# Performance work log

Hardware: AMD Instinct MI355X
Metric: run time of the kernel (lower is better)

The kernel has to match this reference:

```python
import jax, jax.numpy as jnp
import numpy as np

D_MAX = 4                      # max_displacement
OUT_DIM = 2 * D_MAX + 1        # 9 -> 9**3 = 729 displacement offsets


def setup_inputs() -> dict:
    key = jax.random.key(0)
    k1, k2 = jax.random.split(key)
    shape = (1, 32, 48, 48, 48)  # (N, C, H, W, D)
    x1 = jax.random.normal(k1, shape, dtype=jnp.float32)
    x2 = jax.random.normal(k2, shape, dtype=jnp.float32)
    return {"x1": x1, "x2": x2}


def _correlation(x1, x2):
    N, C, H, W, D = x1.shape
    p = D_MAX
    # zero-pad x2 on all three spatial dims (matches F.pad([pad]*6))
    x2p = jnp.pad(x2, ((0, 0), (0, 0), (p, p), (p, p), (p, p)))
    # offsets in the same order as the torch triple loop: i (H) slowest, k (D) fastest
    r = jnp.arange(OUT_DIM)
    offs = jnp.stack(jnp.meshgrid(r, r, r, indexing="ij"), axis=-1).reshape(-1, 3)  # (729, 3)

    def corr_one(o):
        sl = jax.lax.dynamic_slice(x2p, (0, 0, o[0], o[1], o[2]), (N, C, H, W, D))
        return jnp.mean(x1 * sl, axis=1)  # (N, H, W, D) — mean over channels

    cv = jax.vmap(corr_one)(offs)          # (729, N, H, W, D)
    return jnp.transpose(cv, (1, 0, 2, 3, 4))  # (N, 729, H, W, D)


def reference(x1, x2):
    return _correlation(x1, x2)
```

## Files before the change

kernel.cpp:

```cpp
#include <hip/hip_runtime.h>
#include <stdint.h>


#define HH 48
#define WW 48
#define DD 48
#define PAD 4
#define OD 9
#define WT 4
#define PP 8
#define NDG 6
#define CCH 8
#define NCHUNK 4
#define X2ROW 56
#define X2W 12
#define NACT 216
#define X2_UNITS 1344
#define X1_UNITS 384

__global__ __launch_bounds__(256, 2) void corr_kernel(
    const float* __restrict__ x1,
    const float* __restrict__ x2,
    float* __restrict__ out) {

  __shared__ __attribute__((aligned(16))) float s_x2[CCH * X2W * X2ROW];
  __shared__ __attribute__((aligned(16))) float s_x1[CCH * WT * DD];

  const int wt = blockIdx.x;
  const int h  = blockIdx.y;
  const int i  = blockIdx.z;
  const int w0 = wt * WT;
  const int r  = h + i - PAD;
  const int t  = threadIdx.x;
  const bool row_ok = (r >= 0) & (r < HH);

  const bool active = (t < NACT);
  int wl = 0, j = 0, dg = 0;
  if (active) {
    wl = t / (OD * NDG);
    int rem = t - wl * (OD * NDG);
    j = rem / NDG;
    dg = rem - j * NDG;
  }
  const int d0 = dg * PP;

  float acc[OD][PP];
#pragma unroll
  for (int k = 0; k < OD; ++k)
#pragma unroll
    for (int p = 0; p < PP; ++p) acc[k][p] = 0.0f;

  const int rbase = r * (WW * DD);

  for (int ch = 0; ch < NCHUNK; ++ch) {
    const int cbase = ch * CCH;

    float4 v2[6];
#pragma unroll
    for (int u = 0; u < 6; ++u) {
      const int idx = t + u * 256;
      const bool have = (u < 5) || (idx < X2_UNITS);
      const int c   = idx / 168;
      const int rm  = idx - c * 168;
      const int w   = rm / 14;
      const int pos = rm - w * 14;
      const int wg  = w0 + w - PAD;
      float4 val = make_float4(0.f, 0.f, 0.f, 0.f);
      const bool in = have & row_ok & ((unsigned)wg < (unsigned)WW) &
                      ((unsigned)(pos - 1) < 12u);
      if (in) {
        const size_t g = (size_t)(cbase + c) * (HH * WW * DD) + rbase +
                         wg * DD + (pos - 1) * 4;
        val = *reinterpret_cast<const float4*>(x2 + g);
      }
      v2[u] = val;
    }
    float4 v1[2];
#pragma unroll
    for (int u = 0; u < 2; ++u) {
      const int idx = t + u * 256;
      const bool have = (u < 1) || (idx < X1_UNITS);
      float4 val = make_float4(0.f, 0.f, 0.f, 0.f);
      if (have) {
        const int c   = idx / 48;
        const int lin = idx - c * 48;
        const size_t g = (size_t)(cbase + c) * (HH * WW * DD) +
                         (size_t)h * (WW * DD) + w0 * DD + lin * 4;
        val = *reinterpret_cast<const float4*>(x1 + g);
      }
      v1[u] = val;
    }

    __syncthreads();

#pragma unroll
    for (int u = 0; u < 6; ++u) {
      const int idx = t + u * 256;
      if ((u < 5) || (idx < X2_UNITS))
        *reinterpret_cast<float4*>(s_x2 + idx * 4) = v2[u];
    }
#pragma unroll
    for (int u = 0; u < 2; ++u) {
      const int idx = t + u * 256;
      if ((u < 1) || (idx < X1_UNITS))
        *reinterpret_cast<float4*>(s_x1 + idx * 4) = v1[u];
    }
    __syncthreads();

    if (active) {
      for (int c = 0; c < CCH; ++c) {
        float xv[PP];
        const float* px1 = &s_x1[c * (WT * DD) + wl * DD + d0];
#pragma unroll
        for (int p = 0; p < PP; ++p) xv[p] = px1[p];
        float win[PP + 8];
        const float* px2 = &s_x2[c * (X2W * X2ROW) + (wl + j) * X2ROW + d0];
#pragma unroll
        for (int q = 0; q < PP + 8; ++q) win[q] = px2[q];
#pragma unroll
        for (int k = 0; k < OD; ++k)
#pragma unroll
          for (int p = 0; p < PP; ++p)
            acc[k][p] = fmaf(xv[p], win[p + k], acc[k][p]);
      }
    }
  }

  if (active) {
    const float inv = 1.0f / 32.0f;
    const size_t spat = ((size_t)h * WW + (w0 + wl)) * DD + d0;
#pragma unroll
    for (int k = 0; k < OD; ++k) {
      const int o = (i * OD + j) * OD + k;
      float4 lo = make_float4(acc[k][0] * inv, acc[k][1] * inv,
                              acc[k][2] * inv, acc[k][3] * inv);
      float4 hi = make_float4(acc[k][4] * inv, acc[k][5] * inv,
                              acc[k][6] * inv, acc[k][7] * inv);
      float* dst = out + (size_t)o * (HH * WW * DD) + spat;
      *reinterpret_cast<float4*>(dst)     = lo;
      *reinterpret_cast<float4*>(dst + 4) = hi;
    }
  }
}

extern "C" void kernel_launch(void* const* d_in, const int* in_sizes, int n_in,
                              void* d_out, int out_size, void* d_ws, size_t ws_size,
                              hipStream_t stream) {
  const float* x1 = (const float*)d_in[0];
  const float* x2 = (const float*)d_in[1];
  float* out = (float*)d_out;
  dim3 grid(WW / WT, HH, OD);
  corr_kernel<<<grid, 256, 0, stream>>>(x1, x2, out);
}
```

Measured before the change: 395.7 us.

## Prefetch next channel chunk into registers during compute and pad x2 smem rows

Precomputes the per-thread global offsets and validity masks once, then issues the loads for the next channel chunk right after the shared-memory store so they overlap the FMA loop. It also widens the x2 shared-memory row from 56 to 60 floats (15 float4 per row), likely to reduce bank conflicts, and raises launch_bounds min blocks to 3. The risk is higher register pressure from the prefetch buffers plus the tighter register cap, which may cause spills.

```diff
diff --git a/kernel.cpp b/kernel.cpp
--- a/kernel.cpp
+++ b/kernel.cpp
@@ -12,13 +12,16 @@
 #define NDG 6
 #define CCH 8
 #define NCHUNK 4
-#define X2ROW 56
+#define X2ROW 60
+#define X2POS 15
 #define X2W 12
 #define NACT 216
-#define X2_UNITS 1344
+#define X2_UNITS 1440
 #define X1_UNITS 384
+#define HWD (HH * WW * DD)
+#define CHSTRIDE (CCH * HWD)
 
-__global__ __launch_bounds__(256, 2) void corr_kernel(
+__global__ __launch_bounds__(256, 3) void corr_kernel(
     const float* __restrict__ x1,
     const float* __restrict__ x2,
     float* __restrict__ out) {
@@ -44,53 +47,55 @@
   }
   const int d0 = dg * PP;
 
+  const int rbase = r * (WW * DD);
+  uint32_t o2[6];
+  bool in2[6];
+#pragma unroll
+  for (int u = 0; u < 6; ++u) {
+    const int idx = t + u * 256;
+    const bool have = (u < 5) || (idx < X2_UNITS);
+    const int c   = idx / (X2W * X2POS);
+    const int rm  = idx - c * (X2W * X2POS);
+    const int w   = rm / X2POS;
+    const int pos = rm - w * X2POS;
+    const int wg  = w0 + w - PAD;
+    in2[u] = have & row_ok & ((unsigned)wg < (unsigned)WW) &
+             ((unsigned)(pos - 1) < 12u);
+    o2[u] = (uint32_t)(c * HWD + rbase + wg * DD + (pos - 1) * 4);
+  }
+  uint32_t o1[2];
+  bool in1[2];
+#pragma unroll
+  for (int u = 0; u < 2; ++u) {
+    const int idx = t + u * 256;
+    in1[u] = (u < 1) || (idx < X1_UNITS);
+    const int c   = idx / 48;
+    const int lin = idx - c * 48;
+    o1[u] = (uint32_t)(c * HWD + h * (WW * DD) + w0 * DD + lin * 4);
+  }
+
   float acc[OD][PP];
 #pragma unroll
   for (int k = 0; k < OD; ++k)
 #pragma unroll
     for (int p = 0; p < PP; ++p) acc[k][p] = 0.0f;
 
-  const int rbase = r * (WW * DD);
+  float4 v2[6], v1[2];
+#pragma unroll
+  for (int u = 0; u < 6; ++u) {
+    float4 val = make_float4(0.f, 0.f, 0.f, 0.f);
+    if (in2[u]) val = *reinterpret_cast<const float4*>(x2 + o2[u]);
+    v2[u] = val;
+  }
+#pragma unroll
+  for (int u = 0; u < 2; ++u) {
+    float4 val = make_float4(0.f, 0.f, 0.f, 0.f);
+    if (in1[u]) val = *reinterpret_cast<const float4*>(x1 + o1[u]);
+    v1[u] = val;
+  }
 
+#pragma unroll
   for (int ch = 0; ch < NCHUNK; ++ch) {
-    const int cbase = ch * CCH;
-
-    float4 v2[6];
-#pragma unroll
-    for (int u = 0; u < 6; ++u) {
-      const int idx = t + u * 256;
-      const bool have = (u < 5) || (idx < X2_UNITS);
-      const int c   = idx / 168;
-      const int rm  = idx - c * 168;
-      const int w   = rm / 14;
-      const int pos = rm - w * 14;
-      const int wg  = w0 + w - PAD;
-      float4 val = make_float4(0.f, 0.f, 0.f, 0.f);
-      const bool in = have & row_ok & ((unsigned)wg < (unsigned)WW) &
-                      ((unsigned)(pos - 1) < 12u);
-      if (in) {
-        const size_t g = (size_t)(cbase + c) * (HH * WW * DD) + rbase +
-                         wg * DD + (pos - 1) * 4;
-        val = *reinterpret_cast<const float4*>(x2 + g);
-      }
-      v2[u] = val;
-    }
-    float4 v1[2];
-#pragma unroll
-    for (int u = 0; u < 2; ++u) {
-      const int idx = t + u * 256;
-      const bool have = (u < 1) || (idx < X1_UNITS);
-      float4 val = make_float4(0.f, 0.f, 0.f, 0.f);
-      if (have) {
-        const int c   = idx / 48;
-        const int lin = idx - c * 48;
-        const size_t g = (size_t)(cbase + c) * (HH * WW * DD) +
-                         (size_t)h * (WW * DD) + w0 * DD + lin * 4;
-        val = *reinterpret_cast<const float4*>(x1 + g);
-      }
-      v1[u] = val;
-    }
-
     __syncthreads();
 
 #pragma unroll
@@ -106,6 +111,23 @@
         *reinterpret_cast<float4*>(s_x1 + idx * 4) = v1[u];
     }
     __syncthreads();
+
+    if (ch + 1 < NCHUNK) {
+      const float* b2 = x2 + (size_t)(ch + 1) * CHSTRIDE;
+      const float* b1 = x1 + (size_t)(ch + 1) * CHSTRIDE;
+#pragma unroll
+      for (int u = 0; u < 6; ++u) {
+        float4 val = make_float4(0.f, 0.f, 0.f, 0.f);
+        if (in2[u]) val = *reinterpret_cast<const float4*>(b2 + o2[u]);
+        v2[u] = val;
+      }
+#pragma unroll
+      for (int u = 0; u < 2; ++u) {
+        float4 val = make_float4(0.f, 0.f, 0.f, 0.f);
+        if (in1[u]) val = *reinterpret_cast<const float4*>(b1 + o1[u]);
+        v1[u] = val;
+      }
+    }
 
     if (active) {
       for (int c = 0; c < CCH; ++c) {
```

Result: slower. 428.7 us (+8.3%).

## Double-buffer channel chunks via direct global-to-LDS async loads

Applied to the files above, without the earlier changes.

Replaces the register-staged global→LDS copy with AMD global_load_lds direct transfers into a double-buffered shared tile, prefetching the next channel chunk while the current one is computed. Chunk size halves to 4 channels, the shared buffers are zero-filled once so the padding halo stays zero, and hand-placed vmcnt waits plus raw barriers replace __syncthreads. It also widens LDS reads to float4 and raises the occupancy hint to 3 blocks. This aims to hide global load latency and cut register pressure, but relies on tricky manual waitcnt counts and per-wave load mapping.

```diff
diff --git a/kernel.cpp b/kernel.cpp
--- a/kernel.cpp
+++ b/kernel.cpp
@@ -10,21 +10,29 @@
 #define WT 4
 #define PP 8
 #define NDG 6
-#define CCH 8
-#define NCHUNK 4
-#define X2ROW 56
+#define CCH 4
+#define NCHUNK 8
+#define X2POS 15
+#define X2ROW 60
 #define X2W 12
 #define NACT 216
-#define X2_UNITS 1344
-#define X1_UNITS 384
+#define X2_FLOATS (CCH * X2W * X2ROW)
+#define X1_FLOATS (CCH * WT * DD)
+#define HWD (HH * WW * DD)
+#define CHFLOATS (CCH * HWD)
 
-__global__ __launch_bounds__(256, 2) void corr_kernel(
+#define GLOAD16(gp, lp)                                                  \
+  __builtin_amdgcn_global_load_lds(                                      \
+      (const __attribute__((address_space(1))) void*)(gp),               \
+      (__attribute__((address_space(3))) void*)(lp), 16, 0, 0)
+
+__global__ __launch_bounds__(256, 3) void corr_kernel(
     const float* __restrict__ x1,
     const float* __restrict__ x2,
     float* __restrict__ out) {
 
-  __shared__ __attribute__((aligned(16))) float s_x2[CCH * X2W * X2ROW];
-  __shared__ __attribute__((aligned(16))) float s_x1[CCH * WT * DD];
+  __shared__ __attribute__((aligned(16))) float s_x2[2][X2_FLOATS];
+  __shared__ __attribute__((aligned(16))) float s_x1[2][X1_FLOATS];
 
   const int wt = blockIdx.x;
   const int h  = blockIdx.y;
@@ -32,7 +40,38 @@
   const int w0 = wt * WT;
   const int r  = h + i - PAD;
   const int t  = threadIdx.x;
+  const int lane = t & 63;
+  const int wv   = t >> 6;
   const bool row_ok = (r >= 0) & (r < HH);
+
+  {
+    const float4 z = make_float4(0.f, 0.f, 0.f, 0.f);
+    float* p2 = &s_x2[0][0];
+    for (int s = t; s < (2 * X2_FLOATS) / 4; s += 256)
+      reinterpret_cast<float4*>(p2)[s] = z;
+    float* p1 = &s_x1[0][0];
+    for (int s = t; s < (2 * X1_FLOATS) / 4; s += 256)
+      reinterpret_cast<float4*>(p1)[s] = z;
+  }
+
+  uint32_t o2[3];
+  bool m2[3];
+#pragma unroll
+  for (int u = 0; u < 3; ++u) {
+    const int m   = u * 64 + lane;
+    const int w   = m / 15;
+    const int pos = m - w * 15;
+    const int wg  = w0 + w - PAD;
+    m2[u] = (m < 180) & row_ok & ((unsigned)wg < (unsigned)WW) &
+            ((unsigned)(pos - 1) < 12u);
+    o2[u] = (uint32_t)(wv * HWD + r * (WW * DD) + wg * DD + (pos - 1) * 4);
+  }
+  const bool m1 = (lane < 48);
+  const uint32_t o1 = (uint32_t)(wv * HWD + h * (WW * DD) + w0 * DD + lane * 4);
+
+  int nvm = 1;
+#pragma unroll
+  for (int u = 0; u < 3; ++u) nvm += (__ballot(m2[u]) != 0ull) ? 1 : 0;
 
   const bool active = (t < NACT);
   int wl = 0, j = 0, dg = 0;
@@ -50,73 +89,53 @@
 #pragma unroll
     for (int p = 0; p < PP; ++p) acc[k][p] = 0.0f;
 
-  const int rbase = r * (WW * DD);
+  __syncthreads();
+
+#pragma unroll
+  for (int u = 0; u < 3; ++u)
+    if (m2[u]) GLOAD16(x2 + o2[u], &s_x2[0][(wv * 180 + u * 64) * 4]);
+  if (m1) GLOAD16(x1 + o1, &s_x1[0][(wv * 48) * 4]);
 
   for (int ch = 0; ch < NCHUNK; ++ch) {
-    const int cbase = ch * CCH;
-
-    float4 v2[6];
+    const int b = ch & 1;
+    if (ch + 1 < NCHUNK) {
+      const float* g2 = x2 + (size_t)(ch + 1) * CHFLOATS;
+      const float* g1 = x1 + (size_t)(ch + 1) * CHFLOATS;
 #pragma unroll
-    for (int u = 0; u < 6; ++u) {
-      const int idx = t + u * 256;
-      const bool have = (u < 5) || (idx < X2_UNITS);
-      const int c   = idx / 168;
-      const int rm  = idx - c * 168;
-      const int w   = rm / 14;
-      const int pos = rm - w * 14;
-      const int wg  = w0 + w - PAD;
-      float4 val = make_float4(0.f, 0.f, 0.f, 0.f);
-      const bool in = have & row_ok & ((unsigned)wg < (unsigned)WW) &
-                      ((unsigned)(pos - 1) < 12u);
-      if (in) {
-        const size_t g = (size_t)(cbase + c) * (HH * WW * DD) + rbase +
-                         wg * DD + (pos - 1) * 4;
-        val = *reinterpret_cast<const float4*>(x2 + g);
+      for (int u = 0; u < 3; ++u)
+        if (m2[u]) GLOAD16(g2 + o2[u], &s_x2[b ^ 1][(wv * 180 + u * 64) * 4]);
+      if (m1) GLOAD16(g1 + o1, &s_x1[b ^ 1][(wv * 48) * 4]);
+      switch (nvm) {
+        case 4: asm volatile("s_waitcnt vmcnt(4)" ::: "memory"); break;
+        case 3: asm volatile("s_waitcnt vmcnt(3)" ::: "memory"); break;
+        case 2: asm volatile("s_waitcnt vmcnt(2)" ::: "memory"); break;
+        default: asm volatile("s_waitcnt vmcnt(1)" ::: "memory"); break;
       }
-      v2[u] = val;
+    } else {
+      asm volatile("s_waitcnt vmcnt(0)" ::: "memory");
     }
-    float4 v1[2];
-#pragma unroll
-    for (int u = 0; u < 2; ++u) {
-      const int idx = t + u * 256;
-      const bool have = (u < 1) || (idx < X1_UNITS);
-      float4 val = make_float4(0.f, 0.f, 0.f, 0.f);
-      if (have) {
-        const int c   = idx / 48;
-        const int lin = idx - c * 48;
-        const size_t g = (size_t)(cbase + c) * (HH * WW * DD) +
-                         (size_t)h * (WW * DD) + w0 * DD + lin * 4;
-        val = *reinterpret_cast<const float4*>(x1 + g);
-      }
-      v1[u] = val;
-    }
-
-    __syncthreads();
-
-#pragma unroll
-    for (int u = 0; u < 6; ++u) {
-      const int idx = t + u * 256;
-      if ((u < 5) || (idx < X2_UNITS))
-        *reinterpret_cast<float4*>(s_x2 + idx * 4) = v2[u];
-    }
-#pragma unroll
-    for (int u = 0; u < 2; ++u) {
-      const int idx = t + u * 256;
-      if ((u < 1) || (idx < X1_UNITS))
-        *reinterpret_cast<float4*>(s_x1 + idx * 4) = v1[u];
-    }
-    __syncthreads();
+    __builtin_amdgcn_s_barrier();
+    __builtin_amdgcn_sched_barrier(0);
 
     if (active) {
+#pragma unroll
       for (int c = 0; c < CCH; ++c) {
+        const float* px1 = &s_x1[b][c * (WT * DD) + wl * DD + d0];
         float xv[PP];
-        const float* px1 = &s_x1[c * (WT * DD) + wl * DD + d0];
 #pragma unroll
-        for (int p = 0; p < PP; ++p) xv[p] = px1[p];
+        for (int q = 0; q < 2; ++q) {
+          const float4 v = *reinterpret_cast<const float4*>(px1 + q * 4);
+          xv[q * 4 + 0] = v.x; xv[q * 4 + 1] = v.y;
+          xv[q * 4 + 2] = v.z; xv[q * 4 + 3] = v.w;
+        }
+        const float* px2 = &s_x2[b][c * (X2W * X2ROW) + (wl + j) * X2ROW + d0];
         float win[PP + 8];
-        const float* px2 = &s_x2[c * (X2W * X2ROW) + (wl + j) * X2ROW + d0];
 #pragma unroll
-        for (int q = 0; q < PP + 8; ++q) win[q] = px2[q];
+        for (int q = 0; q < 4; ++q) {
+          const float4 v = *reinterpret_cast<const float4*>(px2 + q * 4);
+          win[q * 4 + 0] = v.x; win[q * 4 + 1] = v.y;
+          win[q * 4 + 2] = v.z; win[q * 4 + 3] = v.w;
+        }
 #pragma unroll
         for (int k = 0; k < OD; ++k)
 #pragma unroll
@@ -124,6 +143,9 @@
             acc[k][p] = fmaf(xv[p], win[p + k], acc[k][p]);
       }
     }
+    __builtin_amdgcn_sched_barrier(0);
+    __builtin_amdgcn_s_barrier();
+    __builtin_amdgcn_sched_barrier(0);
   }
 
   if (active) {
```

Result: no change. 400.1 us (+1.1%).
